# Performance work log

Measured on AMD Instinct MI355X. Metric: run time of the kernel, lower is better.

The kernel has to match this reference:

```python
import jax, jax.numpy as jnp
import numpy as np

B, F, H, D, K = 16384, 4096, 512, 64, 512  # batch, feat, hidden, emb_dim, codebook size
M = H // D  # code positions per sample


def _leaky(h):
    return jnp.where(h > 0, h, 0.01 * h)


def setup_inputs() -> dict:
    key = jax.random.key(0)
    ks = jax.random.split(key, 16)
    lin = lambda k, i, o: jax.random.normal(k, (i, o), jnp.float32) * (1.0 / np.sqrt(i))
    return {
        "x": jax.random.uniform(ks[0], (B, F), jnp.float32),
        "We1": lin(ks[1], F, 256), "be1": jnp.zeros((256,), jnp.float32),
        "We2": lin(ks[2], 256, 128), "be2": jnp.zeros((128,), jnp.float32),
        "We3": lin(ks[3], 128, H), "be3": jnp.zeros((H,), jnp.float32),
        "Wd1": lin(ks[4], H, 128), "bd1": jnp.zeros((128,), jnp.float32),
        "Wd2": lin(ks[5], 128, 256), "bd2": jnp.zeros((256,), jnp.float32),
        "Wd3": lin(ks[6], 256, F), "bd3": jnp.zeros((F,), jnp.float32),
        "codebook": jax.random.normal(ks[7], (D, K), jnp.float32) * 0.02,  # (emb_dim, num_embeddings)
    }


def _nearest(z_e, codebook):
    # z_e: (B, D, M); codebook: (D, K). Squared-distance argmin over K.
    x2 = jnp.sum(z_e * z_e, axis=1)                       # (B, M)
    xw = jnp.einsum('bdm,dk->bmk', z_e, codebook)         # (B, M, K)
    w2 = jnp.sum(codebook * codebook, axis=0)             # (K,)
    idx = jnp.argmin(x2[..., None] - 2.0 * xw + w2, axis=-1)  # (B, M)
    quant = jnp.swapaxes(codebook.T[idx], 1, 2)           # (B, D, M)
    return quant, idx


def reference(x, We1, be1, We2, be2, We3, be3, Wd1, bd1, Wd2, bd2, Wd3, bd3, codebook):
    # encoder MLP
    h = _leaky(x @ We1 + be1)
    h = _leaky(h @ We2 + be2)
    h = _leaky(h @ We3 + be3)                             # (B, H)
    z_e = h.reshape(B, D, M)
    # emb(z_e, weight_sg=True): straight-through, weight detached
    quant_sg, idx = _nearest(z_e, jax.lax.stop_gradient(codebook))
    z_q = z_e + jax.lax.stop_gradient(quant_sg - z_e)
    # emb(z_e.detach()): grads (if any) flow to codebook via gather
    emb, _ = _nearest(jax.lax.stop_gradient(z_e), codebook)
    # decoder MLP
    g = _leaky(z_q.reshape(B, H) @ Wd1 + bd1)
    g = _leaky(g @ Wd2 + bd2)
    X_pred = jax.nn.sigmoid(g @ Wd3 + bd3)                # (B, F)
    return idx, z_e, z_q, emb, X_pred
```

## Files before the change

kernel.cpp:

```cpp
#include <hip/hip_runtime.h>
#include <cstdint>
#include <cstddef>


static constexpr int BB = 16384;
static constexpr int TM = 128, TN = 128, TK = 16;

typedef __attribute__((ext_vector_type(8))) short short8;
typedef __attribute__((ext_vector_type(8))) _Float16 half8;
typedef __attribute__((ext_vector_type(4))) float f32x4;

__device__ __forceinline__ unsigned short f2bf(float f) {
    union { float f; uint32_t u; } v; v.f = f;
    uint32_t r = (v.u + 0x7FFFu + ((v.u >> 16) & 1u)) >> 16;
    return (unsigned short)r;
}

__device__ __forceinline__ int bsw(int c) { return c + ((c >> 5) << 2); }

#define GLL16(gp, lp) \
    __builtin_amdgcn_global_load_lds( \
        (const __attribute__((address_space(1))) uint32_t*)(gp), \
        (__attribute__((address_space(3))) uint32_t*)(lp), 16, 0, 0)

__global__ __launch_bounds__(256) void gemm_fp32(
    const float* __restrict__ A, const float* __restrict__ Bm,
    const float* __restrict__ bias, float* __restrict__ C,
    float* __restrict__ part,
    int M, int N, int Kd, int kLen, int act)
{
    __shared__ float As[TK][TM + 4];
    __shared__ float Bs[TK][140];
    const int tid = threadIdx.x;
    const int bm = blockIdx.y * TM;
    const int bn = blockIdx.x * TN;
    const int kStart = blockIdx.z * kLen;
    const int tx = tid & 15;
    const int ty = tid >> 4;

    const int arow = tid >> 2;
    const int acol = (tid & 3) << 2;
    const int brow = tid >> 5;
    const int bcol = (tid & 31) << 2;

    float acc[8][8];
#pragma unroll
    for (int i = 0; i < 8; i++)
#pragma unroll
        for (int j = 0; j < 8; j++) acc[i][j] = 0.f;

    const float* Ap0 = A + (size_t)(bm + arow) * Kd + acol;
    const float* Ap1 = A + (size_t)(bm + arow + 64) * Kd + acol;
    const float* Bp0 = Bm + (size_t)brow * N + bn + bcol;
    const float* Bp1 = Bm + (size_t)(brow + 8) * N + bn + bcol;

    const int pb0 = bsw(bcol);
    const int prb0 = bsw(tx * 8);
    const int prb1 = prb0 + 4;

    for (int k0 = kStart; k0 < kStart + kLen; k0 += TK) {
        const float4 a0 = *(const float4*)(Ap0 + k0);
        const float4 a1 = *(const float4*)(Ap1 + k0);
        const float4 b0 = *(const float4*)(Bp0 + (size_t)k0 * N);
        const float4 b1 = *(const float4*)(Bp1 + (size_t)k0 * N);
        __syncthreads();
        As[acol + 0][arow] = a0.x; As[acol + 1][arow] = a0.y;
        As[acol + 2][arow] = a0.z; As[acol + 3][arow] = a0.w;
        As[acol + 0][arow + 64] = a1.x; As[acol + 1][arow + 64] = a1.y;
        As[acol + 2][arow + 64] = a1.z; As[acol + 3][arow + 64] = a1.w;
        *(float4*)&Bs[brow][pb0]     = b0;
        *(float4*)&Bs[brow + 8][pb0] = b1;
        __syncthreads();
#pragma unroll
        for (int kk = 0; kk < TK; kk++) {
            float a[8], b[8];
            *(float4*)&a[0] = *(const float4*)&As[kk][ty * 8];
            *(float4*)&a[4] = *(const float4*)&As[kk][ty * 8 + 4];
            *(float4*)&b[0] = *(const float4*)&Bs[kk][prb0];
            *(float4*)&b[4] = *(const float4*)&Bs[kk][prb1];
#pragma unroll
            for (int i = 0; i < 8; i++)
#pragma unroll
                for (int j = 0; j < 8; j++)
                    acc[i][j] = fmaf(a[i], b[j], acc[i][j]);
        }
    }

    if (part) {
        float* P = part + (size_t)blockIdx.z * M * N;
#pragma unroll
        for (int i = 0; i < 8; i++) {
            const int row = bm + ty * 8 + i;
            *(float4*)&P[(size_t)row * N + bn + tx * 8]     = *(float4*)&acc[i][0];
            *(float4*)&P[(size_t)row * N + bn + tx * 8 + 4] = *(float4*)&acc[i][4];
        }
        return;
    }

    float bv[8];
#pragma unroll
    for (int j = 0; j < 8; j++) bv[j] = bias[bn + tx * 8 + j];
#pragma unroll
    for (int i = 0; i < 8; i++) {
        const int row = bm + ty * 8 + i;
        float o[8];
#pragma unroll
        for (int j = 0; j < 8; j++) {
            float v = acc[i][j] + bv[j];
            if (act == 0) v = (v > 0.f) ? v : 0.01f * v;
            else          v = 1.0f / (1.0f + __expf(-v));
            o[j] = v;
        }
        *(float4*)&C[(size_t)row * N + bn + tx * 8]     = *(float4*)&o[0];
        *(float4*)&C[(size_t)row * N + bn + tx * 8 + 4] = *(float4*)&o[4];
    }
}

__global__ __launch_bounds__(256) void combine_act(
    const float* __restrict__ part, int S, size_t MN,
    const float* __restrict__ bias, int N,
    float* __restrict__ outF, unsigned short* __restrict__ outB)
{
    const size_t e = ((size_t)blockIdx.x * 256 + threadIdx.x) * 4;
    if (e >= MN) return;
    float4 s = *(const float4*)(part + e);
    for (int i = 1; i < S; i++) {
        const float4 p = *(const float4*)(part + (size_t)i * MN + e);
        s.x += p.x; s.y += p.y; s.z += p.z; s.w += p.w;
    }
    const int col = (int)(e & (size_t)(N - 1));
    const float4 bv = *(const float4*)(bias + col);
    float v0 = s.x + bv.x, v1 = s.y + bv.y, v2 = s.z + bv.z, v3 = s.w + bv.w;
    v0 = (v0 > 0.f) ? v0 : 0.01f * v0;
    v1 = (v1 > 0.f) ? v1 : 0.01f * v1;
    v2 = (v2 > 0.f) ? v2 : 0.01f * v2;
    v3 = (v3 > 0.f) ? v3 : 0.01f * v3;
    if (outF) {
        float4 o; o.x = v0; o.y = v1; o.z = v2; o.w = v3;
        *(float4*)(outF + e) = o;
    } else {
        ushort4 o; o.x = f2bf(v0); o.y = f2bf(v1); o.z = f2bf(v2); o.w = f2bf(v3);
        *(ushort4*)(outB + e) = o;
    }
}

__global__ __launch_bounds__(256) void transpose_cast(
    const float* __restrict__ W, unsigned short* __restrict__ WT, int R, int Cc)
{
    __shared__ float s[32][33];
    const int tx = threadIdx.x & 31, ty = threadIdx.x >> 5;
    const int c0 = blockIdx.x * 32, r0 = blockIdx.y * 32;
#pragma unroll
    for (int i = 0; i < 4; i++)
        s[ty + i * 8][tx] = W[(size_t)(r0 + ty + i * 8) * Cc + c0 + tx];
    __syncthreads();
#pragma unroll
    for (int i = 0; i < 4; i++)
        WT[(size_t)(c0 + ty + i * 8) * R + r0 + tx] = f2bf(s[tx][ty + i * 8]);
}

__global__ __launch_bounds__(256) void transpose_split_f16(
    const float* __restrict__ W, unsigned short* __restrict__ Th,
    unsigned short* __restrict__ Tl, int R, int Cc)
{
    __shared__ float s[32][33];
    const int tx = threadIdx.x & 31, ty = threadIdx.x >> 5;
    const int c0 = blockIdx.x * 32, r0 = blockIdx.y * 32;
#pragma unroll
    for (int i = 0; i < 4; i++)
        s[ty + i * 8][tx] = W[(size_t)(r0 + ty + i * 8) * Cc + c0 + tx];
    __syncthreads();
#pragma unroll
    for (int i = 0; i < 4; i++) {
        const float f = s[tx][ty + i * 8];
        const _Float16 h = (_Float16)f;
        const float fh = (float)h;
        const _Float16 lo = (_Float16)((f - fh) * 4096.0f);
        union { _Float16 hf; unsigned short u; } ch, cl;
        ch.hf = h; cl.hf = lo;
        Th[(size_t)(c0 + ty + i * 8) * R + r0 + tx] = ch.u;
        Tl[(size_t)(c0 + ty + i * 8) * R + r0 + tx] = cl.u;
    }
}

__global__ __launch_bounds__(512, 2) void gemm_f16x2_enc1(
    const float* __restrict__ X,
    const unsigned short* __restrict__ Bh,
    const unsigned short* __restrict__ Bl,
    float* __restrict__ part)
{
    __shared__ short Ah[2][4096];
    __shared__ short Al[2][4096];
    __shared__ short Bhs[2][8192];
    __shared__ short Bls[2][8192];
    const int tid = threadIdx.x;
    const int l = tid & 63, w = tid >> 6;
    const int lm = l & 15, lq = l >> 4;
    const int wm = w >> 2, wn = w & 3;
    const int bm = blockIdx.y * 128;
    const int kStart = blockIdx.z * 2048;

    const float* gA = X + (size_t)(bm + w * 16 + lm) * 4096 + kStart + lq * 8;
    const unsigned short* gBh0 = Bh + (size_t)(w * 16 + lm) * 4096 + kStart + lq * 8;
    const unsigned short* gBh1 = gBh0 + (size_t)128 * 4096;
    const unsigned short* gBl0 = Bl + (size_t)(w * 16 + lm) * 4096 + kStart + lq * 8;
    const unsigned short* gBl1 = gBl0 + (size_t)128 * 4096;

    const int aoff = (w << 9) + (l << 3);
    const int afr = (wm << 11) + (lq << 7) + (lm << 3);
    const int bfr = (wn << 11) + (lq << 7) + (lm << 3);

    f32x4 acc1[4][4], acc2[4][4];
#pragma unroll
    for (int i = 0; i < 4; i++)
#pragma unroll
        for (int j = 0; j < 4; j++) {
            acc1[i][j] = (f32x4){0.f, 0.f, 0.f, 0.f};
            acc2[i][j] = (f32x4){0.f, 0.f, 0.f, 0.f};
        }

    GLL16(gBh0, &Bhs[0][w * 512]);
    GLL16(gBh1, &Bhs[0][(w + 8) * 512]);
    GLL16(gBl0, &Bls[0][w * 512]);
    GLL16(gBl1, &Bls[0][(w + 8) * 512]);
    {
        float fv[8];
        *(float4*)&fv[0] = *(const float4*)(gA);
        *(float4*)&fv[4] = *(const float4*)(gA + 4);
        union { _Float16 h[8]; short8 s; } uh, ul;
#pragma unroll
        for (int e = 0; e < 8; e++) {
            const float f = fv[e];
            const _Float16 h = (_Float16)f;
            const float fh = (float)h;
            uh.h[e] = h;
            ul.h[e] = (_Float16)((f - fh) * 4096.0f);
        }
        *(short8*)&Ah[0][aoff] = uh.s;
        *(short8*)&Al[0][aoff] = ul.s;
    }

    for (int k0 = 0; k0 < 2048; k0 += 32) {
        const int buf = (k0 >> 5) & 1;
        const int nb = buf ^ 1;
        const int kn = k0 + 32;
        __syncthreads();
        float4 a0, a1;
        if (kn < 2048) {
            GLL16(gBh0 + kn, &Bhs[nb][w * 512]);
            GLL16(gBh1 + kn, &Bhs[nb][(w + 8) * 512]);
            GLL16(gBl0 + kn, &Bls[nb][w * 512]);
            GLL16(gBl1 + kn, &Bls[nb][(w + 8) * 512]);
            a0 = *(const float4*)(gA + kn);
            a1 = *(const float4*)(gA + kn + 4);
        }
        half8 ah[4], bh[4];
#pragma unroll
        for (int i = 0; i < 4; i++)
            ah[i] = *(const half8*)&Ah[buf][afr + (i << 9)];
#pragma unroll
        for (int j = 0; j < 4; j++)
            bh[j] = *(const half8*)&Bhs[buf][bfr + (j << 9)];
#pragma unroll
        for (int i = 0; i < 4; i++)
#pragma unroll
            for (int j = 0; j < 4; j++)
                acc1[i][j] = __builtin_amdgcn_mfma_f32_16x16x32_f16(
                    ah[i], bh[j], acc1[i][j], 0, 0, 0);
        half8 bl[4];
#pragma unroll
        for (int j = 0; j < 4; j++)
            bl[j] = *(const half8*)&Bls[buf][bfr + (j << 9)];
#pragma unroll
        for (int i = 0; i < 4; i++)
#pragma unroll
            for (int j = 0; j < 4; j++)
                acc2[i][j] = __builtin_amdgcn_mfma_f32_16x16x32_f16(
                    ah[i], bl[j], acc2[i][j], 0, 0, 0);
        half8 al[4];
#pragma unroll
        for (int i = 0; i < 4; i++)
            al[i] = *(const half8*)&Al[buf][afr + (i << 9)];
#pragma unroll
        for (int i = 0; i < 4; i++)
#pragma unroll
            for (int j = 0; j < 4; j++)
                acc2[i][j] = __builtin_amdgcn_mfma_f32_16x16x32_f16(
                    al[i], bh[j], acc2[i][j], 0, 0, 0);
        if (kn < 2048) {
            float fv[8];
            *(float4*)&fv[0] = a0;
            *(float4*)&fv[4] = a1;
            union { _Float16 h[8]; short8 s; } uh, ul;
#pragma unroll
            for (int e = 0; e < 8; e++) {
                const float f = fv[e];
                const _Float16 h = (_Float16)f;
                const float fh = (float)h;
                uh.h[e] = h;
                ul.h[e] = (_Float16)((f - fh) * 4096.0f);
            }
            *(short8*)&Ah[nb][aoff] = uh.s;
            *(short8*)&Al[nb][aoff] = ul.s;
        }
    }

    float* P = part + (size_t)blockIdx.z * BB * 256;
    const float inv = 0.000244140625f;
#pragma unroll
    for (int i = 0; i < 4; i++)
#pragma unroll
        for (int j = 0; j < 4; j++) {
            const int col = wn * 64 + j * 16 + lm;
#pragma unroll
            for (int r = 0; r < 4; r++) {
                const int row = bm + wm * 64 + i * 16 + lq * 4 + r;
                P[(size_t)row * 256 + col] = acc1[i][j][r] + inv * acc2[i][j][r];
            }
        }
}

__global__ __launch_bounds__(256) void gemm_bf16_dec3(
    const unsigned short* __restrict__ Ag,
    const unsigned short* __restrict__ Bt,
    const float* __restrict__ bias, float* __restrict__ C)
{
    __shared__ short As[4096];
    __shared__ short Bs2[4096];
    const int tid = threadIdx.x;
    const int l = tid & 63, w = tid >> 6;
    const int lm = l & 15, lq = l >> 4;
    const int bm = blockIdx.y * 128, bn = blockIdx.x * 128;
    const int wm = (w >> 1) * 64, wn = (w & 1) * 64;

    const int t0 = w * 2, t1 = w * 2 + 1;
    const unsigned short* ga0 = Ag + (size_t)(bm + t0 * 16 + lm) * 256 + lq * 8;
    const unsigned short* ga1 = Ag + (size_t)(bm + t1 * 16 + lm) * 256 + lq * 8;
    const unsigned short* gb0 = Bt + (size_t)(bn + t0 * 16 + lm) * 256 + lq * 8;
    const unsigned short* gb1 = Bt + (size_t)(bn + t1 * 16 + lm) * 256 + lq * 8;

    f32x4 acc[4][4];
#pragma unroll
    for (int i = 0; i < 4; i++)
#pragma unroll
        for (int j = 0; j < 4; j++) acc[i][j] = (f32x4){0.f, 0.f, 0.f, 0.f};

    for (int k0 = 0; k0 < 256; k0 += 32) {
        __syncthreads();
        GLL16(ga0 + k0, &As[t0 * 512]);
        GLL16(ga1 + k0, &As[t1 * 512]);
        GLL16(gb0 + k0, &Bs2[t0 * 512]);
        GLL16(gb1 + k0, &Bs2[t1 * 512]);
        __syncthreads();
        short8 af[4], bf[4];
#pragma unroll
        for (int i = 0; i < 4; i++)
            af[i] = *(const short8*)&As[((w >> 1) * 4 + i) * 512 + lq * 128 + lm * 8];
#pragma unroll
        for (int j = 0; j < 4; j++)
            bf[j] = *(const short8*)&Bs2[((w & 1) * 4 + j) * 512 + lq * 128 + lm * 8];
#pragma unroll
        for (int i = 0; i < 4; i++)
#pragma unroll
            for (int j = 0; j < 4; j++)
                acc[i][j] = __builtin_amdgcn_mfma_f32_16x16x32_bf16(
                    af[i], bf[j], acc[i][j], 0, 0, 0);
    }

#pragma unroll
    for (int i = 0; i < 4; i++) {
#pragma unroll
        for (int j = 0; j < 4; j++) {
            const int col = bn + wn + j * 16 + lm;
            const float bv = bias[col];
#pragma unroll
            for (int r = 0; r < 4; r++) {
                const int row = bm + wm + i * 16 + lq * 4 + r;
                float v = acc[i][j][r] + bv;
                v = 1.0f / (1.0f + __expf(-v));
                C[(size_t)row * 4096 + col] = v;
            }
        }
    }
}

__global__ __launch_bounds__(512) void vq_argmin(
    const float* __restrict__ ze, const float* __restrict__ cb,
    float* __restrict__ idxf)
{
    __shared__ float cbs[64 * 512];
    __shared__ float As[64][68];
    __shared__ float w2s[512];
    const int tid = threadIdx.x;
    const int p0 = blockIdx.x * 64;

    const float4* cb4 = (const float4*)cb;
    float4* cbs4 = (float4*)cbs;
    for (int i = tid; i < 8192; i += 512) cbs4[i] = cb4[i];

    const float4* ze4 = (const float4*)(ze + (size_t)p0 * 64);
    for (int i = tid; i < 1024; i += 512) {
        float4 v = ze4[i];
        int e = i * 4;
        int bo = e >> 9, r = e & 511;
        int d = r >> 3, m = r & 7;
        *(float4*)&As[d][bo * 8 + m] = v;
    }
    __syncthreads();

    {
        float s = 0.f;
#pragma unroll
        for (int d = 0; d < 64; ++d) { float c = cbs[d * 512 + tid]; s = fmaf(c, c, s); }
        w2s[tid] = s;
    }
    __syncthreads();

    const int tx = tid & 63;
    const int ty = tid >> 6;

    float acc[8][8], x2a[8];
#pragma unroll
    for (int i = 0; i < 8; i++) {
        x2a[i] = 0.f;
#pragma unroll
        for (int j = 0; j < 8; j++) acc[i][j] = 0.f;
    }

#pragma unroll 8
    for (int kk = 0; kk < 64; ++kk) {
        float a[8], b[8];
        *(float4*)&a[0] = *(const float4*)&As[kk][ty * 8];
        *(float4*)&a[4] = *(const float4*)&As[kk][ty * 8 + 4];
        *(float4*)&b[0] = *(const float4*)&cbs[kk * 512 + tx * 8];
        *(float4*)&b[4] = *(const float4*)&cbs[kk * 512 + tx * 8 + 4];
#pragma unroll
        for (int i = 0; i < 8; i++) x2a[i] = fmaf(a[i], a[i], x2a[i]);
#pragma unroll
        for (int i = 0; i < 8; i++)
#pragma unroll
            for (int j = 0; j < 8; j++)
                acc[i][j] = fmaf(a[i], b[j], acc[i][j]);
    }

    float w2v[8];
#pragma unroll
    for (int j = 0; j < 8; j++) w2v[j] = w2s[tx * 8 + j];

#pragma unroll
    for (int i = 0; i < 8; i++) {
        float bd = 3.4e38f; int bk = 1 << 30;
#pragma unroll
        for (int j = 0; j < 8; j++) {
            float dsc = (x2a[i] - 2.0f * acc[i][j]) + w2v[j];
            if (dsc < bd) { bd = dsc; bk = tx * 8 + j; }
        }
        for (int off = 32; off > 0; off >>= 1) {
            float od = __shfl_xor(bd, off);
            int   ok = __shfl_xor(bk, off);
            if (od < bd || (od == bd && ok < bk)) { bd = od; bk = ok; }
        }
        if (tx == i) idxf[p0 + ty * 8 + i] = (float)bk;
    }
}

__global__ __launch_bounds__(256) void vq_gather(
    const float* __restrict__ ze, const float* __restrict__ idxf,
    const float* __restrict__ cb,
    float* __restrict__ zq, float* __restrict__ emb)
{
    const int t = blockIdx.x * 256 + threadIdx.x;
    const int e = t * 4;
    const int b = e >> 9, r = e & 511;
    const int d = r >> 3, m = r & 7;
    const float4 z = *(const float4*)(ze + e);
    float q[4];
#pragma unroll
    for (int c = 0; c < 4; c++) {
        int k = (int)idxf[b * 8 + m + c];
        q[c] = cb[d * 512 + k];
    }
    float4 zq4, em4;
    zq4.x = z.x + (q[0] - z.x); zq4.y = z.y + (q[1] - z.y);
    zq4.z = z.z + (q[2] - z.z); zq4.w = z.w + (q[3] - z.w);
    em4.x = q[0]; em4.y = q[1]; em4.z = q[2]; em4.w = q[3];
    *(float4*)(zq + e) = zq4;
    *(float4*)(emb + e) = em4;
}

extern "C" void kernel_launch(void* const* d_in, const int* in_sizes, int n_in,
                              void* d_out, int out_size, void* d_ws, size_t ws_size,
                              hipStream_t stream)
{
    const float* x   = (const float*)d_in[0];
    const float* We1 = (const float*)d_in[1];
    const float* be1 = (const float*)d_in[2];
    const float* We2 = (const float*)d_in[3];
    const float* be2 = (const float*)d_in[4];
    const float* We3 = (const float*)d_in[5];
    const float* be3 = (const float*)d_in[6];
    const float* Wd1 = (const float*)d_in[7];
    const float* bd1 = (const float*)d_in[8];
    const float* Wd2 = (const float*)d_in[9];
    const float* bd2 = (const float*)d_in[10];
    const float* Wd3 = (const float*)d_in[11];
    const float* bd3 = (const float*)d_in[12];
    const float* cb  = (const float*)d_in[13];

    float* out   = (float*)d_out;
    float* o_idx = out;
    float* o_ze  = o_idx + 131072;
    float* o_zq  = o_ze + 8388608;
    float* o_emb = o_zq + 8388608;
    float* o_X   = o_emb + 8388608;

    float* h1 = (float*)d_ws;
    float* h2 = h1 + (size_t)BB * 256;
    float* g1 = h1;
    unsigned short* g2b = (unsigned short*)(h1 + (size_t)BB * 128);
    unsigned short* WT  = (unsigned short*)h2;

    unsigned short* Bth = (unsigned short*)(o_X + 16777216);
    unsigned short* Btl = Bth + 1048576;

    transpose_split_f16<<<dim3(8, 128), 256, 0, stream>>>(We1, Bth, Btl, 4096, 256);
    gemm_f16x2_enc1<<<dim3(1, 128, 2), 512, 0, stream>>>(x, Bth, Btl, o_X);
    combine_act<<<4096, 256, 0, stream>>>(o_X, 2, (size_t)BB * 256, be1, 256, h1, nullptr);
    gemm_fp32<<<dim3(1, 128, 2), 256, 0, stream>>>(
        h1, We2, nullptr, nullptr, o_X, BB, 128, 256, 128, 0);
    combine_act<<<2048, 256, 0, stream>>>(o_X, 2, (size_t)BB * 128, be2, 128, h2, nullptr);
    gemm_fp32<<<dim3(4, 128, 1), 256, 0, stream>>>(
        h2, We3, be3, o_ze, nullptr, BB, 512, 128, 128, 0);

    vq_argmin<<<dim3(2048), dim3(512), 0, stream>>>(o_ze, cb, o_idx);
    vq_gather<<<dim3(8192), dim3(256), 0, stream>>>(o_ze, o_idx, cb, o_zq, o_emb);

    transpose_cast<<<dim3(128, 8), 256, 0, stream>>>(Wd3, WT, 256, 4096);

    gemm_fp32<<<dim3(1, 128, 4), 256, 0, stream>>>(
        o_zq, Wd1, nullptr, nullptr, o_X, BB, 128, 512, 128, 0);
    combine_act<<<2048, 256, 0, stream>>>(o_X, 4, (size_t)BB * 128, bd1, 128, g1, nullptr);
    gemm_fp32<<<dim3(2, 128, 2), 256, 0, stream>>>(
        g1, Wd2, nullptr, nullptr, o_X, BB, 256, 128, 64, 0);
    combine_act<<<4096, 256, 0, stream>>>(o_X, 2, (size_t)BB * 256, bd2, 256, nullptr, g2b);
    gemm_bf16_dec3<<<dim3(32, 128), 256, 0, stream>>>(g2b, WT, bd3, o_X);
}
```

Before: 1.063 ms.

## Retile enc1 split-f16 GEMM to 64-row blocks with 4 waves

The first encoder GEMM now uses 256-thread blocks covering 64 rows × 256 columns instead of 512-thread blocks covering 128 rows, which doubles the grid along M. Each wave now owns a 64-column slice of B and loads four B row-groups itself, while all waves share the same A tile. The aim is more blocks for better occupancy and load balance across CUs. The cost is that the full 256-column B tile (high and low halves) is re-fetched per 64-row block, which doubles B traffic relative to A.

```diff
diff --git a/kernel.cpp b/kernel.cpp
--- a/kernel.cpp
+++ b/kernel.cpp
@@ -183,32 +183,30 @@
     }
 }
 
-__global__ __launch_bounds__(512, 2) void gemm_f16x2_enc1(
+__global__ __launch_bounds__(256, 2) void gemm_f16x2_enc1(
     const float* __restrict__ X,
     const unsigned short* __restrict__ Bh,
     const unsigned short* __restrict__ Bl,
     float* __restrict__ part)
 {
-    __shared__ short Ah[2][4096];
-    __shared__ short Al[2][4096];
+    __shared__ short Ah[2][2048];
+    __shared__ short Al[2][2048];
     __shared__ short Bhs[2][8192];
     __shared__ short Bls[2][8192];
     const int tid = threadIdx.x;
     const int l = tid & 63, w = tid >> 6;
     const int lm = l & 15, lq = l >> 4;
-    const int wm = w >> 2, wn = w & 3;
-    const int bm = blockIdx.y * 128;
+    const int bm = blockIdx.y * 64;
     const int kStart = blockIdx.z * 2048;
 
     const float* gA = X + (size_t)(bm + w * 16 + lm) * 4096 + kStart + lq * 8;
-    const unsigned short* gBh0 = Bh + (size_t)(w * 16 + lm) * 4096 + kStart + lq * 8;
-    const unsigned short* gBh1 = gBh0 + (size_t)128 * 4096;
-    const unsigned short* gBl0 = Bl + (size_t)(w * 16 + lm) * 4096 + kStart + lq * 8;
-    const unsigned short* gBl1 = gBl0 + (size_t)128 * 4096;
+    const unsigned short* gBh0 = Bh + (size_t)(w * 64 + lm) * 4096 + kStart + lq * 8;
+    const unsigned short* gBl0 = Bl + (size_t)(w * 64 + lm) * 4096 + kStart + lq * 8;
+    const size_t rstep = (size_t)16 * 4096;
 
     const int aoff = (w << 9) + (l << 3);
-    const int afr = (wm << 11) + (lq << 7) + (lm << 3);
-    const int bfr = (wn << 11) + (lq << 7) + (lm << 3);
+    const int fr0 = (lq << 7) + (lm << 3);
+    const int bfrB = (w << 11);
 
     f32x4 acc1[4][4], acc2[4][4];
 #pragma unroll
@@ -219,14 +217,18 @@
             acc2[i][j] = (f32x4){0.f, 0.f, 0.f, 0.f};
         }
 
-    GLL16(gBh0, &Bhs[0][w * 512]);
-    GLL16(gBh1, &Bhs[0][(w + 8) * 512]);
-    GLL16(gBl0, &Bls[0][w * 512]);
-    GLL16(gBl1, &Bls[0][(w + 8) * 512]);
     {
         float fv[8];
         *(float4*)&fv[0] = *(const float4*)(gA);
         *(float4*)&fv[4] = *(const float4*)(gA + 4);
+        GLL16(gBh0,             &Bhs[0][bfrB]);
+        GLL16(gBh0 + rstep,     &Bhs[0][bfrB + 512]);
+        GLL16(gBh0 + 2 * rstep, &Bhs[0][bfrB + 1024]);
+        GLL16(gBh0 + 3 * rstep, &Bhs[0][bfrB + 1536]);
+        GLL16(gBl0,             &Bls[0][bfrB]);
+        GLL16(gBl0 + rstep,     &Bls[0][bfrB + 512]);
+        GLL16(gBl0 + 2 * rstep, &Bls[0][bfrB + 1024]);
+        GLL16(gBl0 + 3 * rstep, &Bls[0][bfrB + 1536]);
         union { _Float16 h[8]; short8 s; } uh, ul;
 #pragma unroll
         for (int e = 0; e < 8; e++) {
@@ -247,20 +249,24 @@
         __syncthreads();
         float4 a0, a1;
         if (kn < 2048) {
-            GLL16(gBh0 + kn, &Bhs[nb][w * 512]);
-            GLL16(gBh1 + kn, &Bhs[nb][(w + 8) * 512]);
-            GLL16(gBl0 + kn, &Bls[nb][w * 512]);
-            GLL16(gBl1 + kn, &Bls[nb][(w + 8) * 512]);
             a0 = *(const float4*)(gA + kn);
             a1 = *(const float4*)(gA + kn + 4);
+            GLL16(gBh0 + kn,             &Bhs[nb][bfrB]);
+            GLL16(gBh0 + kn + rstep,     &Bhs[nb][bfrB + 512]);
+            GLL16(gBh0 + kn + 2 * rstep, &Bhs[nb][bfrB + 1024]);
+            GLL16(gBh0 + kn + 3 * rstep, &Bhs[nb][bfrB + 1536]);
+            GLL16(gBl0 + kn,             &Bls[nb][bfrB]);
+            GLL16(gBl0 + kn + rstep,     &Bls[nb][bfrB + 512]);
+            GLL16(gBl0 + kn + 2 * rstep, &Bls[nb][bfrB + 1024]);
+            GLL16(gBl0 + kn + 3 * rstep, &Bls[nb][bfrB + 1536]);
         }
         half8 ah[4], bh[4];
 #pragma unroll
         for (int i = 0; i < 4; i++)
-            ah[i] = *(const half8*)&Ah[buf][afr + (i << 9)];
+            ah[i] = *(const half8*)&Ah[buf][(i << 9) + fr0];
 #pragma unroll
         for (int j = 0; j < 4; j++)
-            bh[j] = *(const half8*)&Bhs[buf][bfr + (j << 9)];
+            bh[j] = *(const half8*)&Bhs[buf][bfrB + (j << 9) + fr0];
 #pragma unroll
         for (int i = 0; i < 4; i++)
 #pragma unroll
@@ -270,7 +276,7 @@
         half8 bl[4];
 #pragma unroll
         for (int j = 0; j < 4; j++)
-            bl[j] = *(const half8*)&Bls[buf][bfr + (j << 9)];
+            bl[j] = *(const half8*)&Bls[buf][bfrB + (j << 9) + fr0];
 #pragma unroll
         for (int i = 0; i < 4; i++)
 #pragma unroll
@@ -280,7 +286,7 @@
         half8 al[4];
 #pragma unroll
         for (int i = 0; i < 4; i++)
-            al[i] = *(const half8*)&Al[buf][afr + (i << 9)];
+            al[i] = *(const half8*)&Al[buf][(i << 9) + fr0];
 #pragma unroll
         for (int i = 0; i < 4; i++)
 #pragma unroll
@@ -311,10 +317,10 @@
     for (int i = 0; i < 4; i++)
 #pragma unroll
         for (int j = 0; j < 4; j++) {
-            const int col = wn * 64 + j * 16 + lm;
+            const int col = w * 64 + j * 16 + lm;
 #pragma unroll
             for (int r = 0; r < 4; r++) {
-                const int row = bm + wm * 64 + i * 16 + lq * 4 + r;
+                const int row = bm + i * 16 + lq * 4 + r;
                 P[(size_t)row * 256 + col] = acc1[i][j][r] + inv * acc2[i][j][r];
             }
         }
@@ -524,7 +530,7 @@
     unsigned short* Btl = Bth + 1048576;
 
     transpose_split_f16<<<dim3(8, 128), 256, 0, stream>>>(We1, Bth, Btl, 4096, 256);
-    gemm_f16x2_enc1<<<dim3(1, 128, 2), 512, 0, stream>>>(x, Bth, Btl, o_X);
+    gemm_f16x2_enc1<<<dim3(1, 256, 2), 256, 0, stream>>>(x, Bth, Btl, o_X);
     combine_act<<<4096, 256, 0, stream>>>(o_X, 2, (size_t)BB * 256, be1, 256, h1, nullptr);
     gemm_fp32<<<dim3(1, 128, 2), 256, 0, stream>>>(
         h1, We2, nullptr, nullptr, o_X, BB, 128, 256, 128, 0);
```

New measurement: 1.095 ms. +3.1%, slower.
